# Optimization experiments

Measured on AMD Instinct MI355X. Metric: run time of the kernel, lower is better.

## Reference

```python
import jax, jax.numpy as jnp
import numpy as np

B, C, H, W = 8, 4, 768, 768
MIN_SIZE = 50          # unused on the keep_largest=True path, matching the torch module
KEEP_LARGEST = True
INF = H * W + 2        # sentinel label for background pixels


def setup_inputs() -> dict:
    key = jax.random.key(0)
    pred = jax.random.normal(key, (B, C, H, W), dtype=jnp.float32)
    return {"pred": pred}


def _ccl_keep_largest(mask):
    """4-connected components of a (H, W) bool mask; returns float mask of the
    largest component (ties broken by smallest raster-order seed label, matching
    np.argmax over scipy.ndimage.label sizes). Empty mask -> all zeros."""
    idx = jnp.arange(1, H * W + 1, dtype=jnp.int32).reshape(H, W)

    def prop(l):
        # min over 4-neighborhood, restricted to foreground pixels
        p = jnp.pad(l, 1, constant_values=INF)
        n = jnp.minimum(jnp.minimum(p[:-2, 1:-1], p[2:, 1:-1]),
                        jnp.minimum(p[1:-1, :-2], p[1:-1, 2:]))
        return jnp.where(mask, jnp.minimum(l, n), INF)

    l0 = jnp.where(mask, idx, INF)
    l1 = prop(l0)

    def cond(c):
        cur, prev = c
        return jnp.any(cur != prev)

    def body(c):
        cur, _ = c
        return prop(cur), cur

    l, _ = jax.lax.while_loop(cond, body, (l1, l0))
    # fixed point: each foreground pixel holds the min seed index of its component
    labels = jnp.where(mask, l, 0)  # 0 = background

    sizes = jax.ops.segment_sum(jnp.ones(H * W, jnp.int32), labels.ravel(),
                                num_segments=H * W + 1)
    sizes = sizes.at[0].set(0)  # exclude background
    if KEEP_LARGEST:
        largest = jnp.argmax(sizes)
        keep = (labels == largest) & (sizes[largest] > 0)
    else:
        good = sizes >= MIN_SIZE
        keep = good[labels] & (labels > 0)
    return keep.astype(jnp.float32)


def reference(pred):
    pred_labels = jnp.argmax(pred, axis=1)  # (B, H, W)
    classes = jnp.arange(1, C)
    # (B, C-1, H, W) binary masks for classes 1..C-1
    masks = pred_labels[:, None, :, :] == classes[None, :, None, None]
    fg = jax.vmap(_ccl_keep_largest)(masks.reshape(-1, H, W)).reshape(B, C - 1, H, W)
    bg = 1.0 - jnp.clip(fg.sum(axis=1), 0.0, 1.0)
    return jnp.concatenate([bg[:, None], fg], axis=1)  # (B, C, H, W)
```

## Files before the change

kernel.cpp:

```cpp
#include <hip/hip_runtime.h>
#include <stdint.h>


constexpr int BB    = 8;
constexpr int CC    = 4;
constexpr int HH    = 768;
constexpr int WW    = 768;
constexpr int HWP   = HH * WW;
constexpr int NMASK = BB * (CC - 1);
constexpr int TPB   = 256;
constexpr int NBLK  = HWP / TPB;
constexpr int NBLK8 = HWP / (8 * TPB);

constexpr int SLAB_ROWS = 4;
constexpr int SLAB_PIX  = SLAB_ROWS * WW;
constexpr int NSLAB     = HH / SLAB_ROWS;
constexpr int GR_SLAB   = SLAB_PIX / 4;
constexpr int NBOUND    = (NSLAB - 1) * WW;
constexpr int NBLK_BR   = (NBOUND + TPB - 1) / TPB;

constexpr int CSH  = 20;
constexpr int LMSK = (1 << CSH) - 1;
constexpr int LSH  = 12;
constexpr int LLMSK = (1 << LSH) - 1;

__device__ __forceinline__ int findroot(const int* __restrict__ P, int x) {
  int l = P[x] & LMSK;
  while (l != x) { x = l; l = P[x] & LMSK; }
  return x;
}

__device__ __forceinline__ void unite(int* P, int a, int b, int cls) {
  a = findroot(P, a);
  b = findroot(P, b);
  while (a != b) {
    if (a < b) { int t = a; a = b; b = t; }
    int old = atomicMin(&P[a], (cls << CSH) | b);
    if ((old & LMSK) == a) return;
    a = findroot(P, old & LMSK);
    b = findroot(P, b);
  }
}

__global__ void __launch_bounds__(TPB)
k_init(const float* __restrict__ pred, int* __restrict__ parent,
       float* __restrict__ out) {
  __shared__ int lp[SLAB_PIX];
  int s = blockIdx.x;
  int b = blockIdx.y;
  int t = threadIdx.x;
  int lane = t & 63;
  const float4* base = (const float4*)(pred + (size_t)b * CC * HWP);
  int4* cntz = (int4*)(out + (size_t)(b * CC + 1) * HWP);
  int4 z4 = make_int4(0, 0, 0, 0);

  unsigned char am[3][4];
#pragma unroll
  for (int i = 0; i < 3; ++i) {
    int g = s * GR_SLAB + i * TPB + t;
    float4 v0 = base[g];
    float4 v1 = base[(size_t)(HWP / 4) + g];
    float4 v2 = base[(size_t)(HWP / 4) * 2 + g];
    float4 v3 = base[(size_t)(HWP / 4) * 3 + g];
    float c0[4] = {v0.x, v0.y, v0.z, v0.w};
    float c1[4] = {v1.x, v1.y, v1.z, v1.w};
    float c2[4] = {v2.x, v2.y, v2.z, v2.w};
    float c3[4] = {v3.x, v3.y, v3.z, v3.w};
#pragma unroll
    for (int j = 0; j < 4; ++j) {
      float bv = c0[j]; int a = 0;
      if (c1[j] > bv) { bv = c1[j]; a = 1; }
      if (c2[j] > bv) { bv = c2[j]; a = 2; }
      if (c3[j] > bv) { bv = c3[j]; a = 3; }
      am[i][j] = (unsigned char)a;
    }
    cntz[g] = z4;

    int cls0 = am[i][0], cls1 = am[i][1], cls2 = am[i][2], cls3 = am[i][3];
    int c4pk = cls0 | (cls1 << 2) | (cls2 << 4) | (cls3 << 6);
    int prevl = __shfl_up(c4pk, 1) >> 6;
    bool b0 = (lane == 0) || (cls0 != (prevl & 3));
    bool b1 = cls1 != cls0;
    bool b2 = cls2 != cls1;
    bool b3 = cls3 != cls2;
    int lb = b3 ? 3 : (b2 ? 2 : (b1 ? 1 : (b0 ? 0 : -1)));
    int v = (lb >= 0) ? lane * 4 + lb : -1;
#pragma unroll
    for (int off = 1; off < 64; off <<= 1) {
      int o = __shfl_up(v, off);
      if (lane >= off && o > v) v = o;
    }
    int ex = __shfl_up(v, 1);
    int rs0 = b0 ? lane * 4     : ex;
    int rs1 = b1 ? lane * 4 + 1 : rs0;
    int rs2 = b2 ? lane * 4 + 2 : rs1;
    int rs3 = b3 ? lane * 4 + 3 : rs2;
    int seg = i * 1024 + (t >> 6) * 256;
    int l0  = seg + lane * 4;
    int4 iv;
    iv.x = cls0 ? (cls0 << LSH) | (seg + rs0) : -1;
    iv.y = cls1 ? (cls1 << LSH) | (seg + rs1) : -1;
    iv.z = cls2 ? (cls2 << LSH) | (seg + rs2) : -1;
    iv.w = cls3 ? (cls3 << LSH) | (seg + rs3) : -1;
    *(int4*)&lp[l0] = iv;
  }

  auto lfind = [&](int x) {
    int l = lp[x] & LLMSK;
    while (l != x) { x = l; l = lp[x] & LLMSK; }
    return x;
  };
  auto lunite = [&](int a, int c, int cls) {
    a = lfind(a); c = lfind(c);
    while (a != c) {
      if (a < c) { int tmp = a; a = c; c = tmp; }
      int old = atomicMin(&lp[a], (cls << LSH) | c);
      if ((old & LLMSK) == a) return;
      a = lfind(old & LLMSK);
      c = lfind(c);
    }
  };

  __syncthreads();

  if (lane == 0) {
#pragma unroll
    for (int i = 0; i < 3; ++i) {
      int seg = i * 1024 + (t >> 6) * 256;
      int cls = am[i][0];
      if (cls && (seg % WW) != 0) {
        int nv = lp[seg - 1];
        if (nv >= 0 && (nv >> LSH) == cls) lunite(seg, seg - 1, cls);
      }
    }
  }
#pragma unroll
  for (int i = 0; i < 3; ++i) {
    int l0   = (i * TPB + t) * 4;
    int row  = l0 / WW;
    int col0 = l0 - row * WW;
    if (row == SLAB_ROWS - 1) continue;
#pragma unroll
    for (int j = 0; j < 4; ++j) {
      int cls = am[i][j];
      if (!cls) continue;
      int l = l0 + j;
      int nv = lp[l + WW];
      if (nv < 0 || (nv >> LSH) != cls) continue;
      if (col0 + j > 0) {
        int lv = lp[l - 1];
        if (lv >= 0 && (lv >> LSH) == cls) {
          int bv = lp[l + WW - 1];
          if (bv >= 0 && (bv >> LSH) == cls) continue;
        }
      }
      lunite(l, l + WW, cls);
    }
  }
  __syncthreads();
  int gbase = s * SLAB_PIX;
  int* Pb = parent + (size_t)b * HWP;
#pragma unroll
  for (int i = 0; i < 3; ++i) {
    int l0 = (i * TPB + t) * 4;
    int4 pv;
    pv.x = (lp[l0]     >= 0) ? ((lp[l0]     >> LSH) << CSH) | (gbase + lfind(l0))     : -1;
    pv.y = (lp[l0 + 1] >= 0) ? ((lp[l0 + 1] >> LSH) << CSH) | (gbase + lfind(l0 + 1)) : -1;
    pv.z = (lp[l0 + 2] >= 0) ? ((lp[l0 + 2] >> LSH) << CSH) | (gbase + lfind(l0 + 2)) : -1;
    pv.w = (lp[l0 + 3] >= 0) ? ((lp[l0 + 3] >> LSH) << CSH) | (gbase + lfind(l0 + 3)) : -1;
    ((int4*)Pb)[s * GR_SLAB + i * TPB + t] = pv;
  }
}

__global__ void __launch_bounds__(TPB)
k_bridge(int* __restrict__ parent) {
  int bp = blockIdx.x * TPB + threadIdx.x;
  if (bp >= NBOUND) return;
  int* P = parent + (size_t)blockIdx.y * HWP;
  int k = bp / WW;
  int x = bp - k * WW;
  int p = (SLAB_ROWS * k + SLAB_ROWS - 1) * WW + x;
  int pv = P[p], qv = P[p + WW];
  if (pv >= 0 && qv >= 0 && ((pv ^ qv) >> CSH) == 0)
    unite(P, p, p + WW, pv >> CSH);
}

__global__ void __launch_bounds__(TPB)
k_flatten_count(int* __restrict__ parent, float* __restrict__ out,
                unsigned long long* __restrict__ blockmax) {
  int pix = blockIdx.x * TPB + threadIdx.x;
  int b   = blockIdx.y;
  int* P  = parent + (size_t)b * HWP;
  int pv  = P[pix];
  int r = -1, cls = 0;
  if (pv >= 0) {
    cls = pv >> CSH;
    int lbl = pv & LMSK;
    r = (lbl == pix) ? pix : findroot(P, lbl);
    if (r != lbl) P[pix] = (cls << CSH) | r;
  }
  int lane = threadIdx.x & 63;
  int prev = __shfl_up(r, 1);
  bool bound = (lane == 0) || (prev != r);
  unsigned long long lb = __ballot(bound);
  unsigned long long pack = 0ull;
  if (bound && r >= 0) {
    unsigned long long rest = (lane == 63) ? 0ull : (lb >> (lane + 1));
    int nxt = rest ? (lane + 1 + (int)__builtin_ctzll(rest)) : 64;
    int len = nxt - lane;
    uint32_t* cnt = (uint32_t*)(out + (size_t)(b * CC + 1) * HWP);
    uint32_t old = atomicAdd(cnt + r, (uint32_t)len);
    pack = (((unsigned long long)(old + (uint32_t)len)) << 32) |
           (unsigned long long)(0xFFFFFFFFu - (uint32_t)r);
  }
  __shared__ unsigned long long sm[3][TPB / 64];
  int wid = threadIdx.x >> 6;
#pragma unroll
  for (int cm = 0; cm < 3; ++cm) {
    unsigned long long pc = (cls == cm + 1) ? pack : 0ull;
#pragma unroll
    for (int off = 32; off > 0; off >>= 1) {
      unsigned long long o = __shfl_down(pc, off);
      if (o > pc) pc = o;
    }
    if (lane == 0) sm[cm][wid] = pc;
  }
  __syncthreads();
  if (threadIdx.x < 3) {
    int cm = threadIdx.x;
    unsigned long long bm = sm[cm][0];
#pragma unroll
    for (int i = 1; i < TPB / 64; ++i) if (sm[cm][i] > bm) bm = sm[cm][i];
    blockmax[(size_t)(b * 3 + cm) * NBLK + blockIdx.x] = bm;
  }
}

__global__ void __launch_bounds__(TPB)
k_reduce_best(const unsigned long long* __restrict__ blockmax,
              unsigned long long* __restrict__ best) {
  int m = blockIdx.x;
  const unsigned long long* bm = blockmax + (size_t)m * NBLK;
  unsigned long long v = 0ull;
  for (int i = threadIdx.x; i < NBLK; i += TPB) {
    unsigned long long o = bm[i];
    if (o > v) v = o;
  }
#pragma unroll
  for (int off = 32; off > 0; off >>= 1) {
    unsigned long long o = __shfl_down(v, off);
    if (o > v) v = o;
  }
  __shared__ unsigned long long sm[TPB / 64];
  int lane = threadIdx.x & 63, wid = threadIdx.x >> 6;
  if (lane == 0) sm[wid] = v;
  __syncthreads();
  if (threadIdx.x == 0) {
    unsigned long long b0 = sm[0];
#pragma unroll
    for (int i = 1; i < TPB / 64; ++i) if (sm[i] > b0) b0 = sm[i];
    best[m] = b0;
  }
}

__global__ void __launch_bounds__(TPB)
k_final(const int* __restrict__ parent, const unsigned long long* __restrict__ best,
        float* __restrict__ out) {
  int b = blockIdx.y;
  int broot[3];
#pragma unroll
  for (int cm = 0; cm < 3; ++cm) {
    unsigned long long bv = best[b * 3 + cm];
    broot[cm] = (bv >> 32) ? (int)(0xFFFFFFFFu - (uint32_t)bv) : -2;
  }
  const int4* Pb = (const int4*)(parent + (size_t)b * HWP);
  float4* ob = (float4*)(out + (size_t)b * CC * HWP);
#pragma unroll
  for (int h = 0; h < 2; ++h) {
    int g = blockIdx.x * (2 * TPB) + h * TPB + threadIdx.x;
    int4 pv = Pb[g];
    int pvs[4] = {pv.x, pv.y, pv.z, pv.w};
    float4 ch[4];
    float* chf = (float*)ch;
#pragma unroll
    for (int c = 0; c < 4; ++c) ch[c] = make_float4(0.f, 0.f, 0.f, 0.f);
#pragma unroll
    for (int j = 0; j < 4; ++j) {
      int v = pvs[j];
      if (v >= 0) {
        int cls = v >> CSH;
        bool match = (v & LMSK) == broot[cls - 1];
        chf[cls * 4 + j] = match ? 1.f : 0.f;
        chf[j]           = match ? 0.f : 1.f;
      } else {
        chf[j] = 1.f;
      }
    }
#pragma unroll
    for (int c = 0; c < 4; ++c)
      ob[(size_t)(HWP / 4) * c + g] = ch[c];
  }
}

extern "C" void kernel_launch(void* const* d_in, const int* in_sizes, int n_in,
                              void* d_out, int out_size, void* d_ws, size_t ws_size,
                              hipStream_t stream) {
  const float* pred = (const float*)d_in[0];
  float* out = (float*)d_out;

  int* parent = (int*)d_ws;
  unsigned long long* best =
      (unsigned long long*)((char*)d_ws + (size_t)BB * HWP * sizeof(int));
  unsigned long long* blockmax = (unsigned long long*)(out + (size_t)2 * HWP);

  dim3 blk(TPB);
  k_init          <<<dim3(NSLAB, BB),   blk, 0, stream>>>(pred, parent, out);
  k_bridge        <<<dim3(NBLK_BR, BB), blk, 0, stream>>>(parent);
  k_flatten_count <<<dim3(NBLK, BB),    blk, 0, stream>>>(parent, out, blockmax);
  k_reduce_best   <<<dim3(NMASK),       blk, 0, stream>>>(blockmax, best);
  k_final         <<<dim3(NBLK8, BB),   blk, 0, stream>>>(parent, best, out);
}
```

Measured before the change: 221.0 us.

## Coarsen flatten-count blocks and fold best-root reduction into final kernel

```diff
diff --git a/kernel.cpp b/kernel.cpp
--- a/kernel.cpp
+++ b/kernel.cpp
@@ -7,9 +7,7 @@
 constexpr int HH    = 768;
 constexpr int WW    = 768;
 constexpr int HWP   = HH * WW;
-constexpr int NMASK = BB * (CC - 1);
 constexpr int TPB   = 256;
-constexpr int NBLK  = HWP / TPB;
 constexpr int NBLK8 = HWP / (8 * TPB);
 
 constexpr int SLAB_ROWS = 4;
@@ -188,42 +186,50 @@
 __global__ void __launch_bounds__(TPB)
 k_flatten_count(int* __restrict__ parent, float* __restrict__ out,
                 unsigned long long* __restrict__ blockmax) {
-  int pix = blockIdx.x * TPB + threadIdx.x;
   int b   = blockIdx.y;
   int* P  = parent + (size_t)b * HWP;
-  int pv  = P[pix];
-  int r = -1, cls = 0;
-  if (pv >= 0) {
-    cls = pv >> CSH;
-    int lbl = pv & LMSK;
-    r = (lbl == pix) ? pix : findroot(P, lbl);
-    if (r != lbl) P[pix] = (cls << CSH) | r;
-  }
+  uint32_t* cnt = (uint32_t*)(out + (size_t)(b * CC + 1) * HWP);
   int lane = threadIdx.x & 63;
-  int prev = __shfl_up(r, 1);
-  bool bound = (lane == 0) || (prev != r);
-  unsigned long long lb = __ballot(bound);
-  unsigned long long pack = 0ull;
-  if (bound && r >= 0) {
-    unsigned long long rest = (lane == 63) ? 0ull : (lb >> (lane + 1));
-    int nxt = rest ? (lane + 1 + (int)__builtin_ctzll(rest)) : 64;
-    int len = nxt - lane;
-    uint32_t* cnt = (uint32_t*)(out + (size_t)(b * CC + 1) * HWP);
-    uint32_t old = atomicAdd(cnt + r, (uint32_t)len);
-    pack = (((unsigned long long)(old + (uint32_t)len)) << 32) |
-           (unsigned long long)(0xFFFFFFFFu - (uint32_t)r);
+  unsigned long long pc0 = 0ull, pc1 = 0ull, pc2 = 0ull;
+#pragma unroll
+  for (int k2 = 0; k2 < 8; ++k2) {
+    int pix = blockIdx.x * (8 * TPB) + k2 * TPB + threadIdx.x;
+    int pv  = P[pix];
+    int r = -1, cls = 0;
+    if (pv >= 0) {
+      cls = pv >> CSH;
+      int lbl = pv & LMSK;
+      r = (lbl == pix) ? pix : findroot(P, lbl);
+      if (r != lbl) P[pix] = (cls << CSH) | r;
+    }
+    int prev = __shfl_up(r, 1);
+    bool bound = (lane == 0) || (prev != r);
+    unsigned long long lb = __ballot(bound);
+    if (bound && r >= 0) {
+      unsigned long long rest = (lane == 63) ? 0ull : (lb >> (lane + 1));
+      int nxt = rest ? (lane + 1 + (int)__builtin_ctzll(rest)) : 64;
+      int len = nxt - lane;
+      uint32_t old = atomicAdd(cnt + r, (uint32_t)len);
+      unsigned long long pack =
+          (((unsigned long long)(old + (uint32_t)len)) << 32) |
+          (unsigned long long)(0xFFFFFFFFu - (uint32_t)r);
+      if (cls == 1 && pack > pc0) pc0 = pack;
+      if (cls == 2 && pack > pc1) pc1 = pack;
+      if (cls == 3 && pack > pc2) pc2 = pack;
+    }
   }
   __shared__ unsigned long long sm[3][TPB / 64];
   int wid = threadIdx.x >> 6;
+  unsigned long long pcs[3] = {pc0, pc1, pc2};
 #pragma unroll
   for (int cm = 0; cm < 3; ++cm) {
-    unsigned long long pc = (cls == cm + 1) ? pack : 0ull;
+    unsigned long long v = pcs[cm];
 #pragma unroll
     for (int off = 32; off > 0; off >>= 1) {
-      unsigned long long o = __shfl_down(pc, off);
-      if (o > pc) pc = o;
-    }
-    if (lane == 0) sm[cm][wid] = pc;
+      unsigned long long o = __shfl_down(v, off);
+      if (o > v) v = o;
+    }
+    if (lane == 0) sm[cm][wid] = v;
   }
   __syncthreads();
   if (threadIdx.x < 3) {
@@ -231,47 +237,43 @@
     unsigned long long bm = sm[cm][0];
 #pragma unroll
     for (int i = 1; i < TPB / 64; ++i) if (sm[cm][i] > bm) bm = sm[cm][i];
-    blockmax[(size_t)(b * 3 + cm) * NBLK + blockIdx.x] = bm;
+    blockmax[(size_t)(b * 3 + cm) * NBLK8 + blockIdx.x] = bm;
   }
 }
 
 __global__ void __launch_bounds__(TPB)
-k_reduce_best(const unsigned long long* __restrict__ blockmax,
-              unsigned long long* __restrict__ best) {
-  int m = blockIdx.x;
-  const unsigned long long* bm = blockmax + (size_t)m * NBLK;
-  unsigned long long v = 0ull;
-  for (int i = threadIdx.x; i < NBLK; i += TPB) {
-    unsigned long long o = bm[i];
-    if (o > v) v = o;
-  }
-#pragma unroll
-  for (int off = 32; off > 0; off >>= 1) {
-    unsigned long long o = __shfl_down(v, off);
-    if (o > v) v = o;
-  }
-  __shared__ unsigned long long sm[TPB / 64];
-  int lane = threadIdx.x & 63, wid = threadIdx.x >> 6;
-  if (lane == 0) sm[wid] = v;
-  __syncthreads();
-  if (threadIdx.x == 0) {
-    unsigned long long b0 = sm[0];
-#pragma unroll
-    for (int i = 1; i < TPB / 64; ++i) if (sm[i] > b0) b0 = sm[i];
-    best[m] = b0;
-  }
-}
-
-__global__ void __launch_bounds__(TPB)
-k_final(const int* __restrict__ parent, const unsigned long long* __restrict__ best,
+k_final(const int* __restrict__ parent,
+        const unsigned long long* __restrict__ blockmax,
         float* __restrict__ out) {
   int b = blockIdx.y;
-  int broot[3];
+  __shared__ int sbroot[3];
+  __shared__ unsigned long long red[TPB / 64];
+  int lane = threadIdx.x & 63, wid = threadIdx.x >> 6;
 #pragma unroll
   for (int cm = 0; cm < 3; ++cm) {
-    unsigned long long bv = best[b * 3 + cm];
-    broot[cm] = (bv >> 32) ? (int)(0xFFFFFFFFu - (uint32_t)bv) : -2;
-  }
+    const unsigned long long* bm = blockmax + (size_t)(b * 3 + cm) * NBLK8;
+    unsigned long long v = 0ull;
+    for (int i = threadIdx.x; i < NBLK8; i += TPB) {
+      unsigned long long o = bm[i];
+      if (o > v) v = o;
+    }
+#pragma unroll
+    for (int off = 32; off > 0; off >>= 1) {
+      unsigned long long o = __shfl_down(v, off);
+      if (o > v) v = o;
+    }
+    if (lane == 0) red[wid] = v;
+    __syncthreads();
+    if (threadIdx.x == 0) {
+      unsigned long long b0 = red[0];
+#pragma unroll
+      for (int i = 1; i < TPB / 64; ++i) if (red[i] > b0) b0 = red[i];
+      sbroot[cm] = (b0 >> 32) ? (int)(0xFFFFFFFFu - (uint32_t)b0) : -2;
+    }
+    __syncthreads();
+  }
+  int broot[3] = {sbroot[0], sbroot[1], sbroot[2]};
+
   const int4* Pb = (const int4*)(parent + (size_t)b * HWP);
   float4* ob = (float4*)(out + (size_t)b * CC * HWP);
 #pragma unroll
@@ -308,14 +310,12 @@
   float* out = (float*)d_out;
 
   int* parent = (int*)d_ws;
-  unsigned long long* best =
+  unsigned long long* blockmax =
       (unsigned long long*)((char*)d_ws + (size_t)BB * HWP * sizeof(int));
-  unsigned long long* blockmax = (unsigned long long*)(out + (size_t)2 * HWP);
 
   dim3 blk(TPB);
   k_init          <<<dim3(NSLAB, BB),   blk, 0, stream>>>(pred, parent, out);
   k_bridge        <<<dim3(NBLK_BR, BB), blk, 0, stream>>>(parent);
-  k_flatten_count <<<dim3(NBLK, BB),    blk, 0, stream>>>(parent, out, blockmax);
-  k_reduce_best   <<<dim3(NMASK),       blk, 0, stream>>>(blockmax, best);
-  k_final         <<<dim3(NBLK8, BB),   blk, 0, stream>>>(parent, best, out);
-}
+  k_flatten_count <<<dim3(NBLK8, BB),   blk, 0, stream>>>(parent, out, blockmax);
+  k_final         <<<dim3(NBLK8, BB),   blk, 0, stream>>>(parent, blockmax, out);
+}
```

Result: slower. 228.5 us (+3.4%).
